# Optimization experiments

Measured on AMD Instinct MI355X. Metric: run time of the kernel, lower is better.

The kernel has to match this reference:

```python
import jax, jax.numpy as jnp
import numpy as np

NUM_HEADS = 4

def setup_inputs() -> dict:
    key = jax.random.key(0)
    ks = jax.random.split(key, 5)
    B, N, C = 2, 4096, 256
    s = 0.02
    return {
        "x": jax.random.normal(ks[0], (B, N, C), dtype=jnp.float32),
        "qkv_w": jax.random.normal(ks[1], (3 * C, C), dtype=jnp.float32) * s,
        "qkv_b": jax.random.normal(ks[2], (3 * C,), dtype=jnp.float32) * s,
        "out_w": jax.random.normal(ks[3], (C, C), dtype=jnp.float32) * s,
        "out_b": jax.random.normal(ks[4], (C,), dtype=jnp.float32) * s,
    }

def reference(x, qkv_w, qkv_b, out_w, out_b):
    # x: [B, N, C]; manual multi-head self-attention (eval mode, dropout off)
    B, N, C = x.shape
    H = NUM_HEADS
    D = C // H
    qkv = x @ qkv_w.T + qkv_b                      # [B, N, 3C]
    qkv = qkv.reshape(B, N, 3, H, D)
    qkv = jnp.transpose(qkv, (2, 0, 3, 1, 4))      # [3, B, H, N, D]
    q, k, v = qkv[0], qkv[1], qkv[2]
    scale = D ** -0.5
    attn = jnp.einsum('bhnd,bhmd->bhnm', q, k) * scale  # [B, H, N, N]
    attn = jax.nn.softmax(attn, axis=-1)
    out = jnp.einsum('bhnm,bhmd->bhnd', attn, v)   # [B, H, N, D]
    out = jnp.transpose(out, (0, 2, 1, 3)).reshape(B, N, C)
    return out @ out_w.T + out_b
```

## Files before the change

kernel.cpp:

```cpp
#include <hip/hip_runtime.h>

typedef __bf16 bf16x8 __attribute__((ext_vector_type(8)));
typedef float f32x4 __attribute__((ext_vector_type(4)));

#define MFMA_BF16(a, b, c) __builtin_amdgcn_mfma_f32_16x16x32_bf16((a), (b), (c), 0, 0, 0)

#define C1 0.18033688f

static __device__ __forceinline__ unsigned short f2bf(float f) {
    unsigned int u = __float_as_uint(f);
    unsigned int r = (u + 0x7fffu + ((u >> 16) & 1u)) >> 16;
    return (unsigned short)r;
}
static __device__ __forceinline__ float bf2f(unsigned short us) {
    return __uint_as_float(((unsigned int)us) << 16);
}
static __device__ __forceinline__ float exp2_hw(float x) {
    float r;
    asm("v_exp_f32 %0, %1" : "=v"(r) : "v"(x));
    return r;
}
static __device__ __forceinline__ unsigned pack_rh(float a, float b) {
    return __byte_perm(__float_as_uint(a) + 0x8000u, __float_as_uint(b) + 0x8000u, 0x7632);
}
static __device__ __forceinline__ void gload16(const void* g, void* l) {
    __builtin_amdgcn_global_load_lds(
        (const __attribute__((address_space(1))) unsigned int*)g,
        (__attribute__((address_space(3))) unsigned int*)l, 16, 0, 0);
}

static __device__ __forceinline__ void conv_seg8(const void* src, unsigned short* dst, int n,
                                                 int lb, bool f32) {
    const int base = lb * 2048 + (int)threadIdx.x * 8;
    if (base < n) {
        if (f32) {
            const float4 u0 = *(const float4*)((const float*)src + base);
            const float4 u1 = *(const float4*)((const float*)src + base + 4);
            uint4 p;
            p.x = pack_rh(u0.x, u0.y);
            p.y = pack_rh(u0.z, u0.w);
            p.z = pack_rh(u1.x, u1.y);
            p.w = pack_rh(u1.z, u1.w);
            *(uint4*)(dst + base) = p;
        } else {
            *(uint4*)(dst + base) = *(const uint4*)((const unsigned short*)src + base);
        }
    }
}

__global__ __launch_bounds__(256) void convert_kernel(
    const void* __restrict__ x, const void* __restrict__ qw, const void* __restrict__ qb,
    const void* __restrict__ ow, const void* __restrict__ ob,
    unsigned short* __restrict__ xb, unsigned short* __restrict__ qwb,
    unsigned short* __restrict__ qbb, unsigned short* __restrict__ owb,
    unsigned short* __restrict__ obb, int* __restrict__ flag) {
    __shared__ int tot;
    if (threadIdx.x == 0) tot = 0;
    __syncthreads();
    {
        unsigned short v = ((const unsigned short*)x)[threadIdx.x];
        int e = (v >> 7) & 0xFF;
        if (e >= 195) atomicAdd(&tot, 1);
    }
    __syncthreads();
    const bool f32 = (tot >= 8);
    if (blockIdx.x == 0 && threadIdx.x == 0) flag[0] = f32 ? 1 : 0;

    const int bid = blockIdx.x;
    if (bid < 1024)       conv_seg8(x,  xb,  2097152, bid,        f32);
    else if (bid < 1120)  conv_seg8(qw, qwb, 196608,  bid - 1024, f32);
    else if (bid < 1121)  conv_seg8(qb, qbb, 768,     bid - 1120, f32);
    else if (bid < 1153)  conv_seg8(ow, owb, 65536,   bid - 1121, f32);
    else                  conv_seg8(ob, obb, 256,     bid - 1153, f32);
}

template <bool QKV>
__global__ __launch_bounds__(256) void gemm_kernel(
    const unsigned short* __restrict__ A, const unsigned short* __restrict__ W,
    const unsigned short* __restrict__ bias, unsigned short* __restrict__ Cb,
    float* __restrict__ Cf, const int* __restrict__ flag,
    unsigned short* __restrict__ Vt, int Nout) {
    constexpr int K = 256;
    __shared__ __align__(16) char sm[32768];

    const int tid = threadIdx.x;
    const int lane = tid & 63;
    const int wv = tid >> 6;
    const int m16 = lane & 15;
    const int quad = lane >> 4;
    const int bm = blockIdx.x * 64;
    const int bn = blockIdx.y * 64;

    int bgo[2], blo[2];
#pragma unroll
    for (int i = 0; i < 2; i++) {
        const int c = wv * 128 + i * 64 + lane;
        const int r = c >> 3, g = (c & 7) ^ (r & 7);
        bgo[i] = r * (K * 2) + g * 16;
        blo[i] = c * 16;
    }
    int bro[4][2];
#pragma unroll
    for (int t = 0; t < 4; t++)
#pragma unroll
        for (int ks = 0; ks < 2; ks++) {
            const int row = t * 16 + m16;
            bro[t][ks] = row * 64 + ((4 * ks + quad) ^ (m16 & 7)) * 8;
        }

    const char* bg = (const char*)(W + (size_t)bn * K);
    const unsigned short* ap = A + (size_t)(bm + wv * 16 + m16) * K + quad * 8;

#pragma unroll
    for (int kb = 0; kb < 4; kb++)
#pragma unroll
        for (int i = 0; i < 2; i++)
            gload16(bg + kb * 128 + bgo[i], sm + kb * 8192 + blo[i]);
    bf16x8 a[4][2];
#pragma unroll
    for (int kb = 0; kb < 4; kb++)
#pragma unroll
        for (int ks = 0; ks < 2; ks++)
            a[kb][ks] = *(const bf16x8*)(ap + kb * 64 + ks * 32);

    __syncthreads();

    f32x4 acc[4] = {};
#pragma unroll
    for (int kb = 0; kb < 4; kb++) {
        const unsigned short* Blds = (const unsigned short*)(sm + kb * 8192);
#pragma unroll
        for (int ks = 0; ks < 2; ks++)
#pragma unroll
            for (int t = 0; t < 4; t++) {
                const bf16x8 b = *(const bf16x8*)(Blds + bro[t][ks]);
                acc[t] = MFMA_BF16(a[kb][ks], b, acc[t]);
            }
    }

    if (QKV && bn >= 512) {
        __syncthreads();
        unsigned short* tr = (unsigned short*)sm;
        const int lr = wv * 16 + quad * 4;
#pragma unroll
        for (int t = 0; t < 4; t++) {
            const float bv = bf2f(bias[bn + t * 16 + m16]);
            uint2 w;
            w.x = pack_rh(acc[t][0] + bv, acc[t][1] + bv);
            w.y = pack_rh(acc[t][2] + bv, acc[t][3] + bv);
            *(uint2*)&tr[(t * 16 + m16) * 72 + lr] = w;
        }
        __syncthreads();
        const int d = tid >> 2;
        const int ch = (tid & 3) * 16;
        const uint4 o4a = *(const uint4*)&tr[d * 72 + ch];
        const uint4 o4b = *(const uint4*)&tr[d * 72 + ch + 8];
        const int hh = (bn - 512) >> 6;
        const int bb = bm >> 12, n0 = bm & 4095;
        const int nn = n0 + ch;
        const int kt = nn >> 7, koff = nn & 127;
        unsigned short* vdst =
            &Vt[(size_t)(((bb * 4 + hh) * 32 + kt) * 64 + d) * 128 + koff];
        *(uint4*)(vdst) = o4a;
        *(uint4*)(vdst + 8) = o4b;
        return;
    }

    const bool outf = (!QKV) && (flag != nullptr) && (*flag != 0);
    const int row0 = bm + wv * 16 + quad * 4;
#pragma unroll
    for (int t = 0; t < 4; t++) {
        const int col = bn + t * 16 + m16;
        const float bv = bf2f(bias[col]);
        float v[4];
#pragma unroll
        for (int r = 0; r < 4; r++) v[r] = acc[t][r] + bv;
        if (QKV) {
            const float sc = (col < 256) ? C1 : 1.0f;
#pragma unroll
            for (int r = 0; r < 4; r++)
                Cb[(size_t)(row0 + r) * 768 + col] = f2bf(v[r] * sc);
        } else {
            if (outf) {
#pragma unroll
                for (int r = 0; r < 4; r++) Cf[(size_t)(row0 + r) * Nout + col] = v[r];
            } else {
#pragma unroll
                for (int r = 0; r < 4; r++) Cb[(size_t)(row0 + r) * Nout + col] = f2bf(v[r]);
            }
        }
    }
}

#define ZERO_S(S)                                                     \
    do {                                                              \
        _Pragma("unroll") for (int mb = 0; mb < 2; mb++)              \
            _Pragma("unroll") for (int j = 0; j < 4; j++)             \
                S[mb][j] = (f32x4){0.f, 0.f, 0.f, 0.f};               \
    } while (0)

#define QKT(S, KBASE)                                                          \
    do {                                                                       \
        const unsigned short* Kb_ = (const unsigned short*)(KBASE);            \
        __builtin_amdgcn_s_setprio(1);                                         \
        _Pragma("unroll") for (int mb = 0; mb < 2; mb++)                       \
            _Pragma("unroll") for (int ks = 0; ks < 2; ks++) {                 \
                const bf16x8 ka_ = *(const bf16x8*)(Kb_ + kro[mb][ks]);        \
                _Pragma("unroll") for (int j = 0; j < 4; j++)                  \
                    S[mb][j] = MFMA_BF16(ka_, qf[j][ks], S[mb][j]);            \
            }                                                                  \
        __builtin_amdgcn_s_setprio(0);                                         \
    } while (0)

#define EXPP(S, PA)                                                            \
    do {                                                                       \
        _Pragma("unroll") for (int j = 0; j < 4; j++) {                        \
            const float e0 = exp2_hw(S[0][j][0]);                              \
            const float e1 = exp2_hw(S[0][j][1]);                              \
            const float e2 = exp2_hw(S[0][j][2]);                              \
            const float e3 = exp2_hw(S[0][j][3]);                              \
            const float e4 = exp2_hw(S[1][j][0]);                              \
            const float e5 = exp2_hw(S[1][j][1]);                              \
            const float e6 = exp2_hw(S[1][j][2]);                              \
            const float e7 = exp2_hw(S[1][j][3]);                              \
            uint4 pw_;                                                         \
            pw_.x = pack_rh(e0, e1);                                           \
            pw_.y = pack_rh(e2, e3);                                           \
            pw_.z = pack_rh(e4, e5);                                           \
            pw_.w = pack_rh(e6, e7);                                           \
            PA[j] = *(const bf16x8*)&pw_;                                      \
        }                                                                      \
    } while (0)

#define PVACC(PA, VBASE)                                                       \
    do {                                                                       \
        const unsigned short* Vb_ = (const unsigned short*)(VBASE);            \
        __builtin_amdgcn_s_setprio(1);                                         \
        _Pragma("unroll") for (int j = 0; j < 4; j++)                          \
            o1[j] = MFMA_BF16(PA[j], ones, o1[j]);                             \
        _Pragma("unroll") for (int t = 0; t < 4; t++) {                        \
            const uint2 va_ = *(const uint2*)(Vb_ + vroA[t]);                  \
            const uint2 vc_ = *(const uint2*)(Vb_ + (vroA[t] ^ 16));           \
            uint4 vv_;                                                         \
            vv_.x = va_.x;                                                     \
            vv_.y = va_.y;                                                     \
            vv_.z = vc_.x;                                                     \
            vv_.w = vc_.y;                                                     \
            const bf16x8 vb_ = *(const bf16x8*)&vv_;                           \
            _Pragma("unroll") for (int j = 0; j < 4; j++)                      \
                o[j][t] = MFMA_BF16(PA[j], vb_, o[j][t]);                      \
        }                                                                      \
        __builtin_amdgcn_s_setprio(0);                                         \
    } while (0)

#define GLK(DST)                                                               \
    {                                                                          \
        _Pragma("unroll") for (int i = 0; i < 4; i++)                          \
            gload16(kgn + kgo[i], (DST) + klo[i]);                             \
        kgn += 196608;                                                         \
    }
#define GLV(DST)                                                               \
    {                                                                          \
        _Pragma("unroll") for (int i = 0; i < 4; i++)                          \
            gload16(vgn + vgo[i], (DST) + vlo[i]);                             \
        vgn += 16384;                                                          \
    }

__global__ __launch_bounds__(256, 2) void attn_kernel(
    const unsigned short* __restrict__ qkv, const unsigned short* __restrict__ Vt,
    unsigned short* __restrict__ attn, int iters) {
    const int N = 4096, C3 = 768;
    __shared__ __align__(16) char sm[65536];

    const int tid = threadIdx.x;
    const int lane = tid & 63;
    const int wv = tid >> 6;
    const int m16 = lane & 15;
    const int quad = lane >> 4;

    const int bh = blockIdx.x & 7;
    const int qt = blockIdx.x >> 3;
    const int b = bh >> 2, h = bh & 3;

    bf16x8 qf[4][2];
#pragma unroll
    for (int j = 0; j < 4; j++)
#pragma unroll
        for (int ks = 0; ks < 2; ks++)
            qf[j][ks] = *(const bf16x8*)(qkv + ((size_t)b * N + qt * 64 + j * 16 + m16) * C3 +
                                         h * 64 + ks * 32 + quad * 8);

    uint4 ones_u;
    ones_u.x = ones_u.y = ones_u.z = ones_u.w = 0x3F803F80u;
    const bf16x8 ones = *(const bf16x8*)&ones_u;

    int kgo[4], vgo[4], klo[4], vlo[4];
#pragma unroll
    for (int i = 0; i < 4; i++) {
        const int c = i * 64 + lane;
        const int r = c >> 3, g = (c & 7) ^ (r & 7);
        kgo[i] = (wv * 32 + r) * 1536 + g * 16;
        klo[i] = c * 16;
        const int d = c >> 2, js = c & 3, jg = js ^ ((d >> 2) & 3);
        vgo[i] = d * 256 + wv * 64 + jg * 16;
        vlo[i] = c * 16;
    }
    int kro[2][2];
#pragma unroll
    for (int mb = 0; mb < 2; mb++)
#pragma unroll
        for (int ks = 0; ks < 2; ks++) {
            const int row = mb * 16 + m16;
            kro[mb][ks] = row * 64 + ((4 * ks + quad) ^ (m16 & 7)) * 8;
        }
    int vroA[4];
#pragma unroll
    for (int t = 0; t < 4; t++) {
        const int d = t * 16 + m16;
        const int c0 = (quad >> 1) ^ ((d >> 2) & 3);
        vroA[t] = d * 32 + c0 * 8 + (quad & 1) * 4;
    }

    char* Kreg0 = sm + wv * 8192;
    char* Vreg0 = sm + 32768 + wv * 8192;

    const char* kgp = (const char*)(qkv + (size_t)b * N * C3 + 256 + h * 64);
    const char* vgp = (const char*)(Vt + (size_t)bh * 262144);

#pragma unroll
    for (int i = 0; i < 4; i++) gload16(kgp + kgo[i], Kreg0 + klo[i]);
#pragma unroll
    for (int i = 0; i < 4; i++) gload16(vgp + vgo[i], Vreg0 + vlo[i]);
#pragma unroll
    for (int i = 0; i < 4; i++) gload16(kgp + 196608 + kgo[i], Kreg0 + 4096 + klo[i]);
#pragma unroll
    for (int i = 0; i < 4; i++) gload16(vgp + 16384 + vgo[i], Vreg0 + 4096 + vlo[i]);
    const char* kgn = kgp + 2 * 196608;
    const char* vgn = vgp + 2 * 16384;

    f32x4 o[4][4] = {};
    f32x4 o1[4] = {};
    f32x4 sA[2][4], sB[2][4];
    bf16x8 pa[4];

    asm volatile("s_waitcnt vmcnt(12)" ::: "memory");
    ZERO_S(sA);
    QKT(sA, Kreg0);

    for (int t2 = 0; t2 < 15; ++t2) {
        asm volatile("s_waitcnt vmcnt(4)" ::: "memory");
        GLK(Kreg0);
        ZERO_S(sB);
        QKT(sB, Kreg0 + 4096);
        EXPP(sA, pa);
        PVACC(pa, Vreg0);
        asm volatile("s_waitcnt lgkmcnt(0)" ::: "memory");
        GLV(Vreg0);

        asm volatile("s_waitcnt vmcnt(4)" ::: "memory");
        GLK(Kreg0 + 4096);
        ZERO_S(sA);
        QKT(sA, Kreg0);
        EXPP(sB, pa);
        PVACC(pa, Vreg0 + 4096);
        asm volatile("s_waitcnt lgkmcnt(0)" ::: "memory");
        GLV(Vreg0 + 4096);
    }
    asm volatile("s_waitcnt vmcnt(4)" ::: "memory");
    ZERO_S(sB);
    QKT(sB, Kreg0 + 4096);
    EXPP(sA, pa);
    PVACC(pa, Vreg0);
    asm volatile("s_waitcnt vmcnt(0)" ::: "memory");
    EXPP(sB, pa);
    PVACC(pa, Vreg0 + 4096);

    __syncthreads();
    float* Ored = (float*)sm;
    float* lsum = (float*)(sm + 16384);
    if (m16 == 0) {
#pragma unroll
        for (int j = 0; j < 4; j++)
#pragma unroll
            for (int r = 0; r < 4; r++)
                lsum[wv * 64 + j * 16 + quad * 4 + r] = o1[j][r];
    }
    const int row = tid >> 4;
    const int col = (tid & 15) * 4;
#pragma unroll
    for (int j = 0; j < 4; j++) {
#pragma unroll
        for (int t = 0; t < 4; t++)
#pragma unroll
            for (int r = 0; r < 4; r++)
                Ored[(wv * 16 + quad * 4 + r) * 64 + t * 16 + m16] = o[j][t][r];
        __syncthreads();
        f32x4 sum = *(f32x4*)&Ored[row * 64 + col];
        sum += *(f32x4*)&Ored[1024 + row * 64 + col];
        sum += *(f32x4*)&Ored[2048 + row * 64 + col];
        sum += *(f32x4*)&Ored[3072 + row * 64 + col];
        const float lq = lsum[j * 16 + row] + lsum[64 + j * 16 + row] +
                         lsum[128 + j * 16 + row] + lsum[192 + j * 16 + row];
        const int n = qt * 64 + j * 16 + row;
        const float inv = 1.0f / lq;
        uint2 w;
        w.x = pack_rh(sum[0] * inv, sum[1] * inv);
        w.y = pack_rh(sum[2] * inv, sum[3] * inv);
        *(uint2*)&attn[((size_t)b * N + n) * 256 + h * 64 + col] = w;
        __syncthreads();
    }
}

extern "C" void kernel_launch(void* const* d_in, const int* in_sizes, int n_in,
                              void* d_out, int out_size, void* d_ws, size_t ws_size,
                              hipStream_t stream) {
    const int B = 2, N = 4096, H = 4;
    const int M = B * N;

    char* wsb = (char*)d_ws;
    int* flag = (int*)wsb;
    unsigned short* xb      = (unsigned short*)(wsb + 64);
    unsigned short* qwb     = xb + 2097152;
    unsigned short* qbb     = qwb + 196608;
    unsigned short* owb     = qbb + 768;
    unsigned short* obb     = owb + 65536;
    unsigned short* qkv_ws  = obb + 256;
    unsigned short* Vt_ws   = qkv_ws + 6291456;
    unsigned short* attn_ws = Vt_ws + 2097152;

    convert_kernel<<<1154, 256, 0, stream>>>(d_in[0], d_in[1], d_in[2], d_in[3], d_in[4],
                                             xb, qwb, qbb, owb, obb, flag);

    gemm_kernel<true><<<dim3(M / 64, 768 / 64), 256, 0, stream>>>(
        xb, qwb, qbb, qkv_ws, nullptr, nullptr, Vt_ws, 768);

    attn_kernel<<<512, 256, 0, stream>>>(qkv_ws, Vt_ws, attn_ws, 32);

    gemm_kernel<false><<<dim3(M / 64, 256 / 64), 256, 0, stream>>>(
        attn_ws, owb, obb, (unsigned short*)d_out, (float*)d_out, flag, nullptr, 256);
}
```

Measured before the change: 136.1 us.

## Fuse fp32-to-bf16 input conversion into GEMM loads and drop convert kernel

```diff
diff --git a/kernel.cpp b/kernel.cpp
--- a/kernel.cpp
+++ b/kernel.cpp
@@ -29,57 +29,11 @@
         (__attribute__((address_space(3))) unsigned int*)l, 16, 0, 0);
 }
 
-static __device__ __forceinline__ void conv_seg8(const void* src, unsigned short* dst, int n,
-                                                 int lb, bool f32) {
-    const int base = lb * 2048 + (int)threadIdx.x * 8;
-    if (base < n) {
-        if (f32) {
-            const float4 u0 = *(const float4*)((const float*)src + base);
-            const float4 u1 = *(const float4*)((const float*)src + base + 4);
-            uint4 p;
-            p.x = pack_rh(u0.x, u0.y);
-            p.y = pack_rh(u0.z, u0.w);
-            p.z = pack_rh(u1.x, u1.y);
-            p.w = pack_rh(u1.z, u1.w);
-            *(uint4*)(dst + base) = p;
-        } else {
-            *(uint4*)(dst + base) = *(const uint4*)((const unsigned short*)src + base);
-        }
-    }
-}
-
-__global__ __launch_bounds__(256) void convert_kernel(
-    const void* __restrict__ x, const void* __restrict__ qw, const void* __restrict__ qb,
-    const void* __restrict__ ow, const void* __restrict__ ob,
-    unsigned short* __restrict__ xb, unsigned short* __restrict__ qwb,
-    unsigned short* __restrict__ qbb, unsigned short* __restrict__ owb,
-    unsigned short* __restrict__ obb, int* __restrict__ flag) {
-    __shared__ int tot;
-    if (threadIdx.x == 0) tot = 0;
-    __syncthreads();
-    {
-        unsigned short v = ((const unsigned short*)x)[threadIdx.x];
-        int e = (v >> 7) & 0xFF;
-        if (e >= 195) atomicAdd(&tot, 1);
-    }
-    __syncthreads();
-    const bool f32 = (tot >= 8);
-    if (blockIdx.x == 0 && threadIdx.x == 0) flag[0] = f32 ? 1 : 0;
-
-    const int bid = blockIdx.x;
-    if (bid < 1024)       conv_seg8(x,  xb,  2097152, bid,        f32);
-    else if (bid < 1120)  conv_seg8(qw, qwb, 196608,  bid - 1024, f32);
-    else if (bid < 1121)  conv_seg8(qb, qbb, 768,     bid - 1120, f32);
-    else if (bid < 1153)  conv_seg8(ow, owb, 65536,   bid - 1121, f32);
-    else                  conv_seg8(ob, obb, 256,     bid - 1153, f32);
-}
-
 template <bool QKV>
 __global__ __launch_bounds__(256) void gemm_kernel(
-    const unsigned short* __restrict__ A, const unsigned short* __restrict__ W,
-    const unsigned short* __restrict__ bias, unsigned short* __restrict__ Cb,
-    float* __restrict__ Cf, const int* __restrict__ flag,
-    unsigned short* __restrict__ Vt, int Nout) {
+    const void* __restrict__ Av, const void* __restrict__ Wv,
+    const void* __restrict__ biasv, unsigned short* __restrict__ Cb,
+    float* __restrict__ Cf, unsigned short* __restrict__ Vt, int Nout) {
     constexpr int K = 256;
     __shared__ __align__(16) char sm[32768];
 
@@ -91,13 +45,26 @@
     const int bm = blockIdx.x * 64;
     const int bn = blockIdx.y * 64;
 
-    int bgo[2], blo[2];
+    int cnt = 0;
+    {
+        const unsigned short* sw = (const unsigned short*)Wv;
+#pragma unroll
+        for (int i = 0; i < 4; i++) {
+            const int e = (sw[i * 64 + lane] >> 7) & 0xFF;
+            cnt += __popcll(__ballot(e >= 195));
+        }
+    }
+    const bool f32 = (cnt >= 8);
+
+    int bgo[2], blo[2], brow[2], bchk[2];
 #pragma unroll
     for (int i = 0; i < 2; i++) {
         const int c = wv * 128 + i * 64 + lane;
         const int r = c >> 3, g = (c & 7) ^ (r & 7);
         bgo[i] = r * (K * 2) + g * 16;
         blo[i] = c * 16;
+        brow[i] = r;
+        bchk[i] = g;
     }
     int bro[4][2];
 #pragma unroll
@@ -108,20 +75,55 @@
             bro[t][ks] = row * 64 + ((4 * ks + quad) ^ (m16 & 7)) * 8;
         }
 
-    const char* bg = (const char*)(W + (size_t)bn * K);
-    const unsigned short* ap = A + (size_t)(bm + wv * 16 + m16) * K + quad * 8;
-
-#pragma unroll
-    for (int kb = 0; kb < 4; kb++)
-#pragma unroll
-        for (int i = 0; i < 2; i++)
-            gload16(bg + kb * 128 + bgo[i], sm + kb * 8192 + blo[i]);
     bf16x8 a[4][2];
-#pragma unroll
-    for (int kb = 0; kb < 4; kb++)
-#pragma unroll
-        for (int ks = 0; ks < 2; ks++)
-            a[kb][ks] = *(const bf16x8*)(ap + kb * 64 + ks * 32);
+    if (f32) {
+        const float* Wf = (const float*)Wv;
+#pragma unroll
+        for (int kb = 0; kb < 4; kb++)
+#pragma unroll
+            for (int i = 0; i < 2; i++) {
+                const float* src = Wf + (size_t)(bn + brow[i]) * K + kb * 64 + bchk[i] * 8;
+                const float4 u0 = *(const float4*)src;
+                const float4 u1 = *(const float4*)(src + 4);
+                uint4 p;
+                p.x = pack_rh(u0.x, u0.y);
+                p.y = pack_rh(u0.z, u0.w);
+                p.z = pack_rh(u1.x, u1.y);
+                p.w = pack_rh(u1.z, u1.w);
+                *(uint4*)(sm + kb * 8192 + blo[i]) = p;
+            }
+    } else {
+        const char* bg = (const char*)Wv + (size_t)bn * K * 2;
+#pragma unroll
+        for (int kb = 0; kb < 4; kb++)
+#pragma unroll
+            for (int i = 0; i < 2; i++)
+                gload16(bg + kb * 128 + bgo[i], sm + kb * 8192 + blo[i]);
+    }
+    if (QKV && f32) {
+        const float* Af = (const float*)Av + (size_t)(bm + wv * 16 + m16) * K + quad * 8;
+#pragma unroll
+        for (int kb = 0; kb < 4; kb++)
+#pragma unroll
+            for (int ks = 0; ks < 2; ks++) {
+                const float4 u0 = *(const float4*)(Af + kb * 64 + ks * 32);
+                const float4 u1 = *(const float4*)(Af + kb * 64 + ks * 32 + 4);
+                uint4 p;
+                p.x = pack_rh(u0.x, u0.y);
+                p.y = pack_rh(u0.z, u0.w);
+                p.z = pack_rh(u1.x, u1.y);
+                p.w = pack_rh(u1.z, u1.w);
+                a[kb][ks] = *(const bf16x8*)&p;
+            }
+    } else {
+        const unsigned short* ap =
+            (const unsigned short*)Av + (size_t)(bm + wv * 16 + m16) * K + quad * 8;
+#pragma unroll
+        for (int kb = 0; kb < 4; kb++)
+#pragma unroll
+            for (int ks = 0; ks < 2; ks++)
+                a[kb][ks] = *(const bf16x8*)(ap + kb * 64 + ks * 32);
+    }
 
     __syncthreads();
 
@@ -138,13 +140,17 @@
             }
     }
 
+    const float* bf_ = (const float*)biasv;
+    const unsigned short* bh_ = (const unsigned short*)biasv;
+
     if (QKV && bn >= 512) {
         __syncthreads();
         unsigned short* tr = (unsigned short*)sm;
         const int lr = wv * 16 + quad * 4;
 #pragma unroll
         for (int t = 0; t < 4; t++) {
-            const float bv = bf2f(bias[bn + t * 16 + m16]);
+            const int col = bn + t * 16 + m16;
+            const float bv = f32 ? bf_[col] : bf2f(bh_[col]);
             uint2 w;
             w.x = pack_rh(acc[t][0] + bv, acc[t][1] + bv);
             w.y = pack_rh(acc[t][2] + bv, acc[t][3] + bv);
@@ -166,12 +172,11 @@
         return;
     }
 
-    const bool outf = (!QKV) && (flag != nullptr) && (*flag != 0);
     const int row0 = bm + wv * 16 + quad * 4;
 #pragma unroll
     for (int t = 0; t < 4; t++) {
         const int col = bn + t * 16 + m16;
-        const float bv = bf2f(bias[col]);
+        const float bv = f32 ? bf_[col] : bf2f(bh_[col]);
         float v[4];
 #pragma unroll
         for (int r = 0; r < 4; r++) v[r] = acc[t][r] + bv;
@@ -181,7 +186,7 @@
             for (int r = 0; r < 4; r++)
                 Cb[(size_t)(row0 + r) * 768 + col] = f2bf(v[r] * sc);
         } else {
-            if (outf) {
+            if (f32) {
 #pragma unroll
                 for (int r = 0; r < 4; r++) Cf[(size_t)(row0 + r) * Nout + col] = v[r];
             } else {
@@ -418,24 +423,15 @@
     const int M = B * N;
 
     char* wsb = (char*)d_ws;
-    int* flag = (int*)wsb;
-    unsigned short* xb      = (unsigned short*)(wsb + 64);
-    unsigned short* qwb     = xb + 2097152;
-    unsigned short* qbb     = qwb + 196608;
-    unsigned short* owb     = qbb + 768;
-    unsigned short* obb     = owb + 65536;
-    unsigned short* qkv_ws  = obb + 256;
+    unsigned short* qkv_ws  = (unsigned short*)wsb;
     unsigned short* Vt_ws   = qkv_ws + 6291456;
     unsigned short* attn_ws = Vt_ws + 2097152;
 
-    convert_kernel<<<1154, 256, 0, stream>>>(d_in[0], d_in[1], d_in[2], d_in[3], d_in[4],
-                                             xb, qwb, qbb, owb, obb, flag);
-
     gemm_kernel<true><<<dim3(M / 64, 768 / 64), 256, 0, stream>>>(
-        xb, qwb, qbb, qkv_ws, nullptr, nullptr, Vt_ws, 768);
+        d_in[0], d_in[1], d_in[2], qkv_ws, nullptr, Vt_ws, 768);
 
     attn_kernel<<<512, 256, 0, stream>>>(qkv_ws, Vt_ws, attn_ws, 32);
 
     gemm_kernel<false><<<dim3(M / 64, 256 / 64), 256, 0, stream>>>(
-        attn_ws, owb, obb, (unsigned short*)d_out, (float*)d_out, flag, nullptr, 256);
-}
+        attn_ws, d_in[3], d_in[4], (unsigned short*)d_out, (float*)d_out, nullptr, 256);
+}
```

New measurement: 136.1 us. About the same (+0.0%).
